# Kernel optimization log

Measured on AMD Instinct MI355X. Metric: run time of the kernel, lower is better.

Reference implementation:

```python
import jax, jax.numpy as jnp
import numpy as np

M, N = 128, 128          # SOM grid
NITER = 1000             # total training iterations
ALPHA = 0.3              # base learning rate (torch default)
SIGMA = max(M, N) / 2.0  # base neighbourhood radius (torch default)
BS, DIM = 4096, 768


def setup_inputs() -> dict:
    key = jax.random.key(0)
    k1, k2 = jax.random.split(key)
    embedded = jax.random.normal(k1, (BS, DIM), dtype=jnp.float32)   # SapBERT CLS reps
    weights = jax.random.normal(k2, (M * N, DIM), dtype=jnp.float32)  # codebook / SOM weights
    return {"embedded": embedded, "weights": weights, "it": 100}


def reference(embedded, weights, it):
    comps = weights.shape[0]
    # neuron grid locations [comps, 2] (row-major i,j like neuron_locations())
    locs = jnp.stack(
        jnp.meshgrid(jnp.arange(M), jnp.arange(N), indexing="ij"), axis=-1
    ).reshape(comps, 2).astype(jnp.float32)

    # BMU search: squared Euclidean distances (argmin identical to argmin of sqrt)
    # [bs, comps] — avoids materializing the torch [bs, comps, dim] repeat
    d2 = (
        jnp.sum(embedded * embedded, axis=1)[:, None]
        + jnp.sum(weights * weights, axis=1)[None, :]
        - 2.0 * (embedded @ weights.T)
    )
    bmu_index = jnp.argmin(d2, axis=1)          # [bs]
    bmu_loc = locs[bmu_index]                   # [bs, 2] gather

    # linearly decaying learning rate / sigma
    decay = 1.0 - it / NITER
    alpha_op = ALPHA * decay
    sigma_op = SIGMA * decay

    # Gaussian neighbourhood over grid distances [bs, comps]
    grid_d2 = jnp.sum((locs[None, :, :] - bmu_loc[:, None, :]) ** 2, axis=-1)
    lr = alpha_op * jnp.exp(-grid_d2 / (sigma_op * sigma_op))

    # delta[c,d] = sum_b lr[b,c] * (x[b,d] - w[c,d])  (no bs x comps x dim materialization)
    delta = jnp.einsum("bc,bd->cd", lr, embedded) - jnp.sum(lr, axis=0)[:, None] * weights
    return weights + delta
```

## Files before the change

kernel.cpp:

```cpp
#include <hip/hip_runtime.h>
#include <cstdint>
#include <cstddef>

#define BS    4096
#define DIM   768
#define DH    384
#define GM    128
#define GN    128
#define COMPS (GM * GN)
#define NITER_F 1000.0f
#define ALPHA0  0.3f
#define SIGMA0  64.0f

typedef _Float16 half8  __attribute__((ext_vector_type(8)));
typedef _Float16 half4v __attribute__((ext_vector_type(4)));
typedef _Float16 half2v __attribute__((ext_vector_type(2)));
typedef float    floatx4 __attribute__((ext_vector_type(4)));

#define XH_OFF    0UL
#define WH_OFF    (8UL * 1024UL * 1024UL)
#define GQ_OFF    0UL
#define GQ_BYTES  ((size_t)COMPS * DH * 4UL)
#define HQ_OFF    (26UL * 1024UL * 1024UL)
#define ETABH_OFF (44UL * 1024UL * 1024UL)
#define BEST_OFF  ((size_t)COMPS * DIM * 4UL)
#define BEST_BYTES ((size_t)BS * 8UL)
#define CNT_OFF   (BEST_OFF + BEST_BYTES)
#define CNT_BYTES ((size_t)COMPS * 4UL)
#define CNTH_OFF  (CNT_OFF + CNT_BYTES)
#define S_OFF     (CNTH_OFF + CNT_BYTES)
#define ETAB_OFF  (S_OFF + CNT_BYTES)
#define WN2_OFF   (ETAB_OFF + CNT_BYTES)

#define GPTR(p) ((const __attribute__((address_space(1))) void*)(p))
#define LPTR(p) ((__attribute__((address_space(3))) void*)(p))

__device__ __forceinline__ unsigned long long packScore(float s, int c) {
    unsigned u = __float_as_uint(s);
    u = (u & 0x80000000u) ? ~u : (u | 0x80000000u);
    return ((unsigned long long)u << 32) | (unsigned)(~(unsigned)c);
}

__device__ __forceinline__ unsigned long long shfl_xor_u64(unsigned long long v, int m) {
    unsigned lo = (unsigned)v, hi = (unsigned)(v >> 32);
    lo = (unsigned)__shfl_xor((int)lo, m, 64);
    hi = (unsigned)__shfl_xor((int)hi, m, 64);
    return ((unsigned long long)hi << 32) | lo;
}

__global__ void cvt_kernel(const float* __restrict__ src, _Float16* __restrict__ dst, int n4) {
    int i = blockIdx.x * 256 + threadIdx.x;
    if (i >= n4) return;
    float4 v = ((const float4*)src)[i];
    half4v h;
    h[0] = (_Float16)v.x; h[1] = (_Float16)v.y;
    h[2] = (_Float16)v.z; h[3] = (_Float16)v.w;
    ((half4v*)dst)[i] = h;
}

__global__ __launch_bounds__(192) void cvtw_wn2_kernel(
    const float* __restrict__ w, _Float16* __restrict__ wh, float* __restrict__ wn2) {
    const int c = blockIdx.x;
    const int t = threadIdx.x;
    const size_t i4 = (size_t)c * 192 + t;
    float4 v = ((const float4*)w)[i4];
    half4v h;
    h[0] = (_Float16)v.x; h[1] = (_Float16)v.y;
    h[2] = (_Float16)v.z; h[3] = (_Float16)v.w;
    ((half4v*)wh)[i4] = h;
    float s = v.x * v.x + v.y * v.y + v.z * v.z + v.w * v.w;
    #pragma unroll
    for (int off = 32; off; off >>= 1) s += __shfl_down(s, off, 64);
    __shared__ float p[3];
    if ((t & 63) == 0) p[t >> 6] = s;
    __syncthreads();
    if (t == 0) wn2[c] = 0.5f * (p[0] + p[1] + p[2]);
}

__global__ void etab_kernel(const int* __restrict__ itp, float* __restrict__ etab,
                            _Float16* __restrict__ etab_h) {
    const int idx = blockIdx.x * 256 + threadIdx.x;
    const int p = idx >> 7, r = idx & 127;
    const float decay = 1.f - (float)(*itp) / NITER_F;
    const float sig = SIGMA0 * decay;
    const float d = (float)(p - r);
    const float v = expf(-(d * d) / (sig * sig));
    etab[idx] = v;
    etab_h[idx] = (_Float16)v;
}

__global__ __launch_bounds__(256) void bmu_kernel(
    const _Float16* __restrict__ xh, const _Float16* __restrict__ wh,
    const float* __restrict__ wn2, unsigned long long* __restrict__ best) {
    __shared__ _Float16 xs[128 * 32];
    __shared__ _Float16 wsd[128 * 32];
    __shared__ unsigned long long red[128];

    const int tid  = threadIdx.x;
    const int wv   = tid >> 6;
    const int lane = tid & 63;
    const int c0 = blockIdx.x * 128;
    const int b0 = blockIdx.y * 128;

    if (tid < 128) red[tid] = 0ULL;

    floatx4 acc[4][4];
    #pragma unroll
    for (int i = 0; i < 4; ++i)
        #pragma unroll
        for (int j = 0; j < 4; ++j) acc[i][j] = (floatx4){0.f, 0.f, 0.f, 0.f};

    const int rr   = lane >> 2;
    const int pq   = lane & 3;
    const int kk   = pq ^ ((rr >> 1) & 3);
    const int lk   = kk * 8;
    const int q    = lane >> 4;
    const int l15  = lane & 15;
    const int mrow = (wv >> 1) * 64;
    const int ncol = (wv & 1) * 64;

    for (int k0 = 0; k0 < DIM; k0 += 32) {
        #pragma unroll
        for (int s = 0; s < 2; ++s) {
            const int sub = 2 * wv + s;
            const _Float16* gx = xh + (size_t)(b0 + sub * 16 + rr) * DIM + k0 + lk;
            __builtin_amdgcn_global_load_lds(GPTR(gx), LPTR(xs + sub * 512), 16, 0, 0);
            const _Float16* gw = wh + (size_t)(c0 + sub * 16 + rr) * DIM + k0 + lk;
            __builtin_amdgcn_global_load_lds(GPTR(gw), LPTR(wsd + sub * 512), 16, 0, 0);
        }
        __syncthreads();

        half8 af[4], bf[4];
        #pragma unroll
        for (int i = 0; i < 4; ++i) {
            const int row = mrow + i * 16 + l15;
            af[i] = *(const half8*)(xs + row * 32 + (q ^ ((row >> 1) & 3)) * 8);
        }
        #pragma unroll
        for (int j = 0; j < 4; ++j) {
            const int row = ncol + j * 16 + l15;
            bf[j] = *(const half8*)(wsd + row * 32 + (q ^ ((row >> 1) & 3)) * 8);
        }
        #pragma unroll
        for (int i = 0; i < 4; ++i)
            #pragma unroll
            for (int j = 0; j < 4; ++j)
                acc[i][j] = __builtin_amdgcn_mfma_f32_16x16x32_f16(af[i], bf[j], acc[i][j], 0, 0, 0);
        __syncthreads();
    }

    float wnj[4];
    #pragma unroll
    for (int j = 0; j < 4; ++j) wnj[j] = wn2[c0 + ncol + j * 16 + l15];

    #pragma unroll
    for (int i = 0; i < 4; ++i) {
        #pragma unroll
        for (int r = 0; r < 4; ++r) {
            unsigned long long m = 0ULL;
            #pragma unroll
            for (int j = 0; j < 4; ++j) {
                float s = acc[i][j][r] - wnj[j];
                unsigned long long p = packScore(s, c0 + ncol + j * 16 + l15);
                if (p > m) m = p;
            }
            #pragma unroll
            for (int msk = 1; msk <= 8; msk <<= 1) {
                unsigned long long o = shfl_xor_u64(m, msk);
                if (o > m) m = o;
            }
            if (l15 == 0)
                atomicMax(&red[mrow + i * 16 + q * 4 + r], m);
        }
    }
    __syncthreads();
    if (tid < 128) atomicMax(&best[b0 + tid], red[tid]);
}

__global__ void scatter_kernel(const unsigned long long* __restrict__ best,
                               const float* __restrict__ x,
                               float* __restrict__ Gq, float* __restrict__ cnt,
                               int h, int addcnt) {
    const int b = blockIdx.x;
    const int c = (int)(~(unsigned)(best[b] & 0xFFFFFFFFULL));
    float* gr = Gq + (size_t)c * DH;
    const float* xr = x + (size_t)b * DIM + h * DH;
    for (int d = threadIdx.x; d < DH; d += 128) atomicAdd(&gr[d], xr[d]);
    if (threadIdx.x == 0 && addcnt) atomicAdd(&cnt[c], 1.0f);
}

#define EP 136
#define BP 40

__global__ __launch_bounds__(256) void convA_kernel(
    const float* __restrict__ Gq, _Float16* __restrict__ H,
    const _Float16* __restrict__ eh) {
    __shared__ _Float16 Es[128 * EP];
    __shared__ _Float16 Bs[128 * BP];
    const int dt = blockIdx.x;
    const int ib = blockIdx.y;
    const int d0 = dt * 128;
    const int tid = threadIdx.x;
    const int wv = tid >> 6, lane = tid & 63;
    const int l15 = lane & 15, q = lane >> 4;
    const int mrow = (wv >> 1) * 64, ncol = (wv & 1) * 64;

    {
        const int row = tid >> 1, hh = tid & 1;
        const _Float16* src = eh + row * 128 + hh * 64;
        _Float16* dst = Es + row * EP + hh * 64;
        #pragma unroll
        for (int u = 0; u < 8; ++u) *(half8*)(dst + u * 8) = *(const half8*)(src + u * 8);
    }

    floatx4 acc[4][4];
    #pragma unroll
    for (int i = 0; i < 4; ++i)
        #pragma unroll
        for (int j = 0; j < 4; ++j) acc[i][j] = (floatx4){0.f, 0.f, 0.f, 0.f};

    const int jj2 = (tid & 15) * 2;
    const int dd  = (tid >> 4) * 8;
    for (int k0 = 0; k0 < 128; k0 += 32) {
        __syncthreads();
        {
            const float* r0 = Gq + (size_t)(ib * 128 + k0 + jj2) * DH + d0 + dd;
            const float* r1 = r0 + DH;
            float4 a0 = *(const float4*)r0, a1 = *(const float4*)(r0 + 4);
            float4 b0 = *(const float4*)r1, b1 = *(const float4*)(r1 + 4);
            float va[8] = {a0.x, a0.y, a0.z, a0.w, a1.x, a1.y, a1.z, a1.w};
            float vb[8] = {b0.x, b0.y, b0.z, b0.w, b1.x, b1.y, b1.z, b1.w};
            #pragma unroll
            for (int u = 0; u < 8; ++u)
                *(half2v*)(Bs + (dd + u) * BP + jj2) = (half2v){(_Float16)va[u], (_Float16)vb[u]};
        }
        __syncthreads();
        half8 af[4], bf[4];
        #pragma unroll
        for (int i = 0; i < 4; ++i)
            af[i] = *(const half8*)(Es + (mrow + i * 16 + l15) * EP + k0 + q * 8);
        #pragma unroll
        for (int j = 0; j < 4; ++j)
            bf[j] = *(const half8*)(Bs + (ncol + j * 16 + l15) * BP + q * 8);
        #pragma unroll
        for (int i = 0; i < 4; ++i)
            #pragma unroll
            for (int j = 0; j < 4; ++j)
                acc[i][j] = __builtin_amdgcn_mfma_f32_16x16x32_f16(af[i], bf[j], acc[i][j], 0, 0, 0);
    }
    __syncthreads();
    #pragma unroll
    for (int i = 0; i < 4; ++i)
        #pragma unroll
        for (int j = 0; j < 4; ++j)
            #pragma unroll
            for (int r = 0; r < 4; ++r)
                Es[(mrow + i * 16 + q * 4 + r) * EP + ncol + j * 16 + l15] = (_Float16)acc[i][j][r];
    __syncthreads();
    {
        const int row = tid >> 1, hh = tid & 1;
        const _Float16* src = Es + row * EP + hh * 64;
        _Float16* dst = H + ((size_t)ib * 128 + row) * DH + d0 + hh * 64;
        #pragma unroll
        for (int u = 0; u < 8; ++u) *(half8*)(dst + u * 8) = *(const half8*)(src + u * 8);
    }
}

__global__ __launch_bounds__(256) void convB_kernel(
    const _Float16* __restrict__ H, const float* __restrict__ w,
    const float* __restrict__ S, const _Float16* __restrict__ eh,
    const int* __restrict__ itp, float* __restrict__ out, int h) {
    __shared__ _Float16 Es[128 * EP];
    __shared__ _Float16 Bs[128 * BP];
    const int dt = blockIdx.x;
    const int jc = blockIdx.y;
    const int d0 = dt * 128;
    const int tid = threadIdx.x;
    const int wv = tid >> 6, lane = tid & 63;
    const int l15 = lane & 15, q = lane >> 4;
    const int mrow = (wv >> 1) * 64, ncol = (wv & 1) * 64;
    const float alpha = ALPHA0 * (1.f - (float)(*itp) / NITER_F);

    {
        const int row = tid >> 1, hh = tid & 1;
        const _Float16* src = eh + row * 128 + hh * 64;
        _Float16* dst = Es + row * EP + hh * 64;
        #pragma unroll
        for (int u = 0; u < 8; ++u) *(half8*)(dst + u * 8) = *(const half8*)(src + u * 8);
    }

    floatx4 acc[4][4];
    #pragma unroll
    for (int i = 0; i < 4; ++i)
        #pragma unroll
        for (int j = 0; j < 4; ++j) acc[i][j] = (floatx4){0.f, 0.f, 0.f, 0.f};

    const int jj2 = (tid & 15) * 2;
    const int dd  = (tid >> 4) * 8;
    for (int k0 = 0; k0 < 128; k0 += 32) {
        __syncthreads();
        {
            const _Float16* r0 = H + ((size_t)(k0 + jj2) * 128 + jc) * DH + d0 + dd;
            const _Float16* r1 = r0 + (size_t)128 * DH;
            half8 a = *(const half8*)r0;
            half8 b = *(const half8*)r1;
            #pragma unroll
            for (int u = 0; u < 8; ++u)
                *(half2v*)(Bs + (dd + u) * BP + jj2) = (half2v){a[u], b[u]};
        }
        __syncthreads();
        half8 af[4], bf[4];
        #pragma unroll
        for (int i = 0; i < 4; ++i)
            af[i] = *(const half8*)(Es + (mrow + i * 16 + l15) * EP + k0 + q * 8);
        #pragma unroll
        for (int j = 0; j < 4; ++j)
            bf[j] = *(const half8*)(Bs + (ncol + j * 16 + l15) * BP + q * 8);
        #pragma unroll
        for (int i = 0; i < 4; ++i)
            #pragma unroll
            for (int j = 0; j < 4; ++j)
                acc[i][j] = __builtin_amdgcn_mfma_f32_16x16x32_f16(af[i], bf[j], acc[i][j], 0, 0, 0);
    }
    __syncthreads();
    float* Ebf = (float*)Es;
    #pragma unroll
    for (int ch = 0; ch < 2; ++ch) {
        if ((wv >> 1) == ch) {
            #pragma unroll
            for (int i = 0; i < 4; ++i)
                #pragma unroll
                for (int j = 0; j < 4; ++j)
                    #pragma unroll
                    for (int r = 0; r < 4; ++r)
                        Ebf[(i * 16 + q * 4 + r) * 132 + ncol + j * 16 + l15] = acc[i][j][r];
        }
        __syncthreads();
        {
            const int row = tid >> 2, seg = tid & 3;
            const int m = ch * 64 + row;
            const int c = m * 128 + jc;
            const float scl = 1.f - alpha * S[c];
            const size_t g = (size_t)c * DIM + h * DH + d0 + seg * 32;
            #pragma unroll
            for (int u = 0; u < 8; ++u) {
                float4 wv4 = *(const float4*)(w + g + u * 4);
                float4 t4  = *(const float4*)(Ebf + row * 132 + seg * 32 + u * 4);
                float4 o;
                o.x = wv4.x * scl + alpha * t4.x;
                o.y = wv4.y * scl + alpha * t4.y;
                o.z = wv4.z * scl + alpha * t4.z;
                o.w = wv4.w * scl + alpha * t4.w;
                *(float4*)(out + g + u * 4) = o;
            }
        }
        __syncthreads();
    }
}

__global__ void cntconv1(const float* __restrict__ cnt, const float* __restrict__ etab,
                         float* __restrict__ cntH) {
    const int idx = blockIdx.x * 256 + threadIdx.x;
    const int i = idx >> 7, jc = idx & 127;
    float s = 0.f;
    for (int j = 0; j < 128; ++j) s += etab[jc * 128 + j] * cnt[i * 128 + j];
    cntH[idx] = s;
}
__global__ void cntconv2(const float* __restrict__ cntH, const float* __restrict__ etab,
                         float* __restrict__ S) {
    const int idx = blockIdx.x * 256 + threadIdx.x;
    const int ic = idx >> 7, jc = idx & 127;
    float s = 0.f;
    for (int i = 0; i < 128; ++i) s += etab[ic * 128 + i] * cntH[i * 128 + jc];
    S[idx] = s;
}

extern "C" void kernel_launch(void* const* d_in, const int* in_sizes, int n_in,
                              void* d_out, int out_size, void* d_ws, size_t ws_size,
                              hipStream_t stream) {
    const float* x  = (const float*)d_in[0];
    const float* w  = (const float*)d_in[1];
    const int* itp  = (const int*)d_in[2];
    float* out = (float*)d_out;
    char* ws = (char*)d_ws;

    _Float16* xh = (_Float16*)(ws + XH_OFF);
    _Float16* wh = (_Float16*)(ws + WH_OFF);
    float*    Gq = (float*)(ws + GQ_OFF);
    _Float16* Hq = (_Float16*)(ws + HQ_OFF);
    _Float16* eh = (_Float16*)(ws + ETABH_OFF);
    unsigned long long* best = (unsigned long long*)(ws + BEST_OFF);
    float* cnt  = (float*)(ws + CNT_OFF);
    float* cntH = (float*)(ws + CNTH_OFF);
    float* S    = (float*)(ws + S_OFF);
    float* etab = (float*)(ws + ETAB_OFF);
    float* wn2  = (float*)(ws + WN2_OFF);

    hipMemsetAsync(ws + BEST_OFF, 0, BEST_BYTES + CNT_BYTES, stream);

    cvt_kernel<<<(BS * DIM / 4 + 255) / 256, 256, 0, stream>>>(x, xh, BS * DIM / 4);
    cvtw_wn2_kernel<<<COMPS, 192, 0, stream>>>(w, wh, wn2);
    etab_kernel<<<COMPS / 256, 256, 0, stream>>>(itp, etab, eh);

    bmu_kernel<<<dim3(COMPS / 128, BS / 128), 256, 0, stream>>>(xh, wh, wn2, best);

    for (int h = 0; h < 2; ++h) {
        hipMemsetAsync(ws + GQ_OFF, 0, GQ_BYTES, stream);
        scatter_kernel<<<BS, 128, 0, stream>>>(best, x, Gq, cnt, h, h == 0 ? 1 : 0);
        if (h == 0) {
            cntconv1<<<COMPS / 256, 256, 0, stream>>>(cnt, etab, cntH);
            cntconv2<<<COMPS / 256, 256, 0, stream>>>(cntH, etab, S);
        }
        convA_kernel<<<dim3(3, 128), 256, 0, stream>>>(Gq, Hq, eh);
        convB_kernel<<<dim3(3, 128), 256, 0, stream>>>(Hq, w, S, eh, itp, out, h);
    }
}
```

Measured before the change: 360.7 us.

## Process full feature dimension in one pass and compute Gaussian table inline

Replaces the two half-dimension passes (scatter, convA, convB per half) with a single pass over all 768 features, accumulating G at full width and using the output buffer as fp32 scratch for the intermediate H. The etab kernel is removed and the Gaussian neighbourhood weights are recomputed with __expf inside convA, convB and the count convolutions. This cuts launches and memsets and doubles the grid width per convolution. In exchange, H is stored in fp32 instead of fp16, doubling its traffic, and convB reads and writes the same buffer, which relies on each block reading only its own column rows before overwriting them.

```diff
diff --git a/kernel.cpp b/kernel.cpp
--- a/kernel.cpp
+++ b/kernel.cpp
@@ -4,7 +4,6 @@
 
 #define BS    4096
 #define DIM   768
-#define DH    384
 #define GM    128
 #define GN    128
 #define COMPS (GM * GN)
@@ -19,18 +18,15 @@
 
 #define XH_OFF    0UL
 #define WH_OFF    (8UL * 1024UL * 1024UL)
-#define GQ_OFF    0UL
-#define GQ_BYTES  ((size_t)COMPS * DH * 4UL)
-#define HQ_OFF    (26UL * 1024UL * 1024UL)
-#define ETABH_OFF (44UL * 1024UL * 1024UL)
-#define BEST_OFF  ((size_t)COMPS * DIM * 4UL)
+#define G_OFF     0UL
+#define G_BYTES   ((size_t)COMPS * DIM * 4UL)
+#define BEST_OFF  G_BYTES
 #define BEST_BYTES ((size_t)BS * 8UL)
 #define CNT_OFF   (BEST_OFF + BEST_BYTES)
 #define CNT_BYTES ((size_t)COMPS * 4UL)
 #define CNTH_OFF  (CNT_OFF + CNT_BYTES)
 #define S_OFF     (CNTH_OFF + CNT_BYTES)
-#define ETAB_OFF  (S_OFF + CNT_BYTES)
-#define WN2_OFF   (ETAB_OFF + CNT_BYTES)
+#define WN2_OFF   (S_OFF + CNT_BYTES)
 
 #define GPTR(p) ((const __attribute__((address_space(1))) void*)(p))
 #define LPTR(p) ((__attribute__((address_space(3))) void*)(p))
@@ -77,18 +73,6 @@
     if (t == 0) wn2[c] = 0.5f * (p[0] + p[1] + p[2]);
 }
 
-__global__ void etab_kernel(const int* __restrict__ itp, float* __restrict__ etab,
-                            _Float16* __restrict__ etab_h) {
-    const int idx = blockIdx.x * 256 + threadIdx.x;
-    const int p = idx >> 7, r = idx & 127;
-    const float decay = 1.f - (float)(*itp) / NITER_F;
-    const float sig = SIGMA0 * decay;
-    const float d = (float)(p - r);
-    const float v = expf(-(d * d) / (sig * sig));
-    etab[idx] = v;
-    etab_h[idx] = (_Float16)v;
-}
-
 __global__ __launch_bounds__(256) void bmu_kernel(
     const _Float16* __restrict__ xh, const _Float16* __restrict__ wh,
     const float* __restrict__ wn2, unsigned long long* __restrict__ best) {
@@ -179,38 +163,44 @@
 
 __global__ void scatter_kernel(const unsigned long long* __restrict__ best,
                                const float* __restrict__ x,
-                               float* __restrict__ Gq, float* __restrict__ cnt,
-                               int h, int addcnt) {
+                               float* __restrict__ G, float* __restrict__ cnt) {
     const int b = blockIdx.x;
     const int c = (int)(~(unsigned)(best[b] & 0xFFFFFFFFULL));
-    float* gr = Gq + (size_t)c * DH;
-    const float* xr = x + (size_t)b * DIM + h * DH;
-    for (int d = threadIdx.x; d < DH; d += 128) atomicAdd(&gr[d], xr[d]);
-    if (threadIdx.x == 0 && addcnt) atomicAdd(&cnt[c], 1.0f);
+    float* gr = G + (size_t)c * DIM;
+    const float* xr = x + (size_t)b * DIM;
+    #pragma unroll
+    for (int u = 0; u < 3; ++u) {
+        const int d = threadIdx.x + u * 256;
+        atomicAdd(&gr[d], xr[d]);
+    }
+    if (threadIdx.x == 0) atomicAdd(&cnt[c], 1.0f);
 }
 
 #define EP 136
 #define BP 40
 
 __global__ __launch_bounds__(256) void convA_kernel(
-    const float* __restrict__ Gq, _Float16* __restrict__ H,
-    const _Float16* __restrict__ eh) {
+    const float* __restrict__ G, float* __restrict__ H, const int* __restrict__ itp) {
     __shared__ _Float16 Es[128 * EP];
     __shared__ _Float16 Bs[128 * BP];
-    const int dt = blockIdx.x;
+    const int d0 = blockIdx.x * 128;
     const int ib = blockIdx.y;
-    const int d0 = dt * 128;
     const int tid = threadIdx.x;
     const int wv = tid >> 6, lane = tid & 63;
     const int l15 = lane & 15, q = lane >> 4;
     const int mrow = (wv >> 1) * 64, ncol = (wv & 1) * 64;
 
     {
+        const float decay = 1.f - (float)(*itp) / NITER_F;
+        const float sig = SIGMA0 * decay;
+        const float inv = -1.f / (sig * sig);
         const int row = tid >> 1, hh = tid & 1;
-        const _Float16* src = eh + row * 128 + hh * 64;
         _Float16* dst = Es + row * EP + hh * 64;
         #pragma unroll
-        for (int u = 0; u < 8; ++u) *(half8*)(dst + u * 8) = *(const half8*)(src + u * 8);
+        for (int u = 0; u < 64; ++u) {
+            const float dd = (float)(row - hh * 64 - u);
+            dst[u] = (_Float16)__expf(dd * dd * inv);
+        }
     }
 
     floatx4 acc[4][4];
@@ -224,8 +214,8 @@
     for (int k0 = 0; k0 < 128; k0 += 32) {
         __syncthreads();
         {
-            const float* r0 = Gq + (size_t)(ib * 128 + k0 + jj2) * DH + d0 + dd;
-            const float* r1 = r0 + DH;
+            const float* r0 = G + (size_t)(ib * 128 + k0 + jj2) * DIM + d0 + dd;
+            const float* r1 = r0 + DIM;
             float4 a0 = *(const float4*)r0, a1 = *(const float4*)(r0 + 4);
             float4 b0 = *(const float4*)r1, b1 = *(const float4*)(r1 + 4);
             float va[8] = {a0.x, a0.y, a0.z, a0.w, a1.x, a1.y, a1.z, a1.w};
@@ -233,80 +223,6 @@
             #pragma unroll
             for (int u = 0; u < 8; ++u)
                 *(half2v*)(Bs + (dd + u) * BP + jj2) = (half2v){(_Float16)va[u], (_Float16)vb[u]};
-        }
-        __syncthreads();
-        half8 af[4], bf[4];
-        #pragma unroll
-        for (int i = 0; i < 4; ++i)
-            af[i] = *(const half8*)(Es + (mrow + i * 16 + l15) * EP + k0 + q * 8);
-        #pragma unroll
-        for (int j = 0; j < 4; ++j)
-            bf[j] = *(const half8*)(Bs + (ncol + j * 16 + l15) * BP + q * 8);
-        #pragma unroll
-        for (int i = 0; i < 4; ++i)
-            #pragma unroll
-            for (int j = 0; j < 4; ++j)
-                acc[i][j] = __builtin_amdgcn_mfma_f32_16x16x32_f16(af[i], bf[j], acc[i][j], 0, 0, 0);
-    }
-    __syncthreads();
-    #pragma unroll
-    for (int i = 0; i < 4; ++i)
-        #pragma unroll
-        for (int j = 0; j < 4; ++j)
-            #pragma unroll
-            for (int r = 0; r < 4; ++r)
-                Es[(mrow + i * 16 + q * 4 + r) * EP + ncol + j * 16 + l15] = (_Float16)acc[i][j][r];
-    __syncthreads();
-    {
-        const int row = tid >> 1, hh = tid & 1;
-        const _Float16* src = Es + row * EP + hh * 64;
-        _Float16* dst = H + ((size_t)ib * 128 + row) * DH + d0 + hh * 64;
-        #pragma unroll
-        for (int u = 0; u < 8; ++u) *(half8*)(dst + u * 8) = *(const half8*)(src + u * 8);
-    }
-}
-
-__global__ __launch_bounds__(256) void convB_kernel(
-    const _Float16* __restrict__ H, const float* __restrict__ w,
-    const float* __restrict__ S, const _Float16* __restrict__ eh,
-    const int* __restrict__ itp, float* __restrict__ out, int h) {
-    __shared__ _Float16 Es[128 * EP];
-    __shared__ _Float16 Bs[128 * BP];
-    const int dt = blockIdx.x;
-    const int jc = blockIdx.y;
-    const int d0 = dt * 128;
-    const int tid = threadIdx.x;
-    const int wv = tid >> 6, lane = tid & 63;
-    const int l15 = lane & 15, q = lane >> 4;
-    const int mrow = (wv >> 1) * 64, ncol = (wv & 1) * 64;
-    const float alpha = ALPHA0 * (1.f - (float)(*itp) / NITER_F);
-
-    {
-        const int row = tid >> 1, hh = tid & 1;
-        const _Float16* src = eh + row * 128 + hh * 64;
-        _Float16* dst = Es + row * EP + hh * 64;
-        #pragma unroll
-        for (int u = 0; u < 8; ++u) *(half8*)(dst + u * 8) = *(const half8*)(src + u * 8);
-    }
-
-    floatx4 acc[4][4];
-    #pragma unroll
-    for (int i = 0; i < 4; ++i)
-        #pragma unroll
-        for (int j = 0; j < 4; ++j) acc[i][j] = (floatx4){0.f, 0.f, 0.f, 0.f};
-
-    const int jj2 = (tid & 15) * 2;
-    const int dd  = (tid >> 4) * 8;
-    for (int k0 = 0; k0 < 128; k0 += 32) {
-        __syncthreads();
-        {
-            const _Float16* r0 = H + ((size_t)(k0 + jj2) * 128 + jc) * DH + d0 + dd;
-            const _Float16* r1 = r0 + (size_t)128 * DH;
-            half8 a = *(const half8*)r0;
-            half8 b = *(const half8*)r1;
-            #pragma unroll
-            for (int u = 0; u < 8; ++u)
-                *(half2v*)(Bs + (dd + u) * BP + jj2) = (half2v){a[u], b[u]};
         }
         __syncthreads();
         half8 af[4], bf[4];
@@ -339,9 +255,96 @@
         {
             const int row = tid >> 2, seg = tid & 3;
             const int m = ch * 64 + row;
+            const size_t g = (size_t)(ib * 128 + m) * DIM + d0 + seg * 32;
+            #pragma unroll
+            for (int u = 0; u < 8; ++u)
+                *(float4*)(H + g + u * 4) = *(const float4*)(Ebf + row * 132 + seg * 32 + u * 4);
+        }
+        __syncthreads();
+    }
+}
+
+__global__ __launch_bounds__(256) void convB_kernel(
+    const float* H, const float* __restrict__ w,
+    const float* __restrict__ S, const int* __restrict__ itp, float* out) {
+    __shared__ _Float16 Es[128 * EP];
+    __shared__ _Float16 Bs[128 * BP];
+    const int d0 = blockIdx.x * 128;
+    const int jc = blockIdx.y;
+    const int tid = threadIdx.x;
+    const int wv = tid >> 6, lane = tid & 63;
+    const int l15 = lane & 15, q = lane >> 4;
+    const int mrow = (wv >> 1) * 64, ncol = (wv & 1) * 64;
+    const float alpha = ALPHA0 * (1.f - (float)(*itp) / NITER_F);
+
+    {
+        const float decay = 1.f - (float)(*itp) / NITER_F;
+        const float sig = SIGMA0 * decay;
+        const float inv = -1.f / (sig * sig);
+        const int row = tid >> 1, hh = tid & 1;
+        _Float16* dst = Es + row * EP + hh * 64;
+        #pragma unroll
+        for (int u = 0; u < 64; ++u) {
+            const float dd = (float)(row - hh * 64 - u);
+            dst[u] = (_Float16)__expf(dd * dd * inv);
+        }
+    }
+
+    floatx4 acc[4][4];
+    #pragma unroll
+    for (int i = 0; i < 4; ++i)
+        #pragma unroll
+        for (int j = 0; j < 4; ++j) acc[i][j] = (floatx4){0.f, 0.f, 0.f, 0.f};
+
+    const int jj2 = (tid & 15) * 2;
+    const int dd  = (tid >> 4) * 8;
+    for (int k0 = 0; k0 < 128; k0 += 32) {
+        __syncthreads();
+        {
+            const float* r0 = H + (size_t)((k0 + jj2) * 128 + jc) * DIM + d0 + dd;
+            const float* r1 = r0 + (size_t)128 * DIM;
+            float4 a0 = *(const float4*)r0, a1 = *(const float4*)(r0 + 4);
+            float4 b0 = *(const float4*)r1, b1 = *(const float4*)(r1 + 4);
+            float va[8] = {a0.x, a0.y, a0.z, a0.w, a1.x, a1.y, a1.z, a1.w};
+            float vb[8] = {b0.x, b0.y, b0.z, b0.w, b1.x, b1.y, b1.z, b1.w};
+            #pragma unroll
+            for (int u = 0; u < 8; ++u)
+                *(half2v*)(Bs + (dd + u) * BP + jj2) = (half2v){(_Float16)va[u], (_Float16)vb[u]};
+        }
+        __syncthreads();
+        half8 af[4], bf[4];
+        #pragma unroll
+        for (int i = 0; i < 4; ++i)
+            af[i] = *(const half8*)(Es + (mrow + i * 16 + l15) * EP + k0 + q * 8);
+        #pragma unroll
+        for (int j = 0; j < 4; ++j)
+            bf[j] = *(const half8*)(Bs + (ncol + j * 16 + l15) * BP + q * 8);
+        #pragma unroll
+        for (int i = 0; i < 4; ++i)
+            #pragma unroll
+            for (int j = 0; j < 4; ++j)
+                acc[i][j] = __builtin_amdgcn_mfma_f32_16x16x32_f16(af[i], bf[j], acc[i][j], 0, 0, 0);
+    }
+    __syncthreads();
+    float* Ebf = (float*)Es;
+    #pragma unroll
+    for (int ch = 0; ch < 2; ++ch) {
+        if ((wv >> 1) == ch) {
+            #pragma unroll
+            for (int i = 0; i < 4; ++i)
+                #pragma unroll
+                for (int j = 0; j < 4; ++j)
+                    #pragma unroll
+                    for (int r = 0; r < 4; ++r)
+                        Ebf[(i * 16 + q * 4 + r) * 132 + ncol + j * 16 + l15] = acc[i][j][r];
+        }
+        __syncthreads();
+        {
+            const int row = tid >> 2, seg = tid & 3;
+            const int m = ch * 64 + row;
             const int c = m * 128 + jc;
             const float scl = 1.f - alpha * S[c];
-            const size_t g = (size_t)c * DIM + h * DH + d0 + seg * 32;
+            const size_t g = (size_t)c * DIM + d0 + seg * 32;
             #pragma unroll
             for (int u = 0; u < 8; ++u) {
                 float4 wv4 = *(const float4*)(w + g + u * 4);
@@ -358,20 +361,32 @@
     }
 }
 
-__global__ void cntconv1(const float* __restrict__ cnt, const float* __restrict__ etab,
-                         float* __restrict__ cntH) {
+__global__ void cntconv1(const float* __restrict__ cnt, float* __restrict__ cntH,
+                         const int* __restrict__ itp) {
     const int idx = blockIdx.x * 256 + threadIdx.x;
     const int i = idx >> 7, jc = idx & 127;
+    const float decay = 1.f - (float)(*itp) / NITER_F;
+    const float sig = SIGMA0 * decay;
+    const float inv = -1.f / (sig * sig);
     float s = 0.f;
-    for (int j = 0; j < 128; ++j) s += etab[jc * 128 + j] * cnt[i * 128 + j];
+    for (int j = 0; j < 128; ++j) {
+        const float dd = (float)(jc - j);
+        s += __expf(dd * dd * inv) * cnt[i * 128 + j];
+    }
     cntH[idx] = s;
 }
-__global__ void cntconv2(const float* __restrict__ cntH, const float* __restrict__ etab,
-                         float* __restrict__ S) {
+__global__ void cntconv2(const float* __restrict__ cntH, float* __restrict__ S,
+                         const int* __restrict__ itp) {
     const int idx = blockIdx.x * 256 + threadIdx.x;
     const int ic = idx >> 7, jc = idx & 127;
+    const float decay = 1.f - (float)(*itp) / NITER_F;
+    const float sig = SIGMA0 * decay;
+    const float inv = -1.f / (sig * sig);
     float s = 0.f;
-    for (int i = 0; i < 128; ++i) s += etab[ic * 128 + i] * cntH[i * 128 + jc];
+    for (int i = 0; i < 128; ++i) {
+        const float dd = (float)(ic - i);
+        s += __expf(dd * dd * inv) * cntH[i * 128 + jc];
+    }
     S[idx] = s;
 }
 
@@ -386,32 +401,26 @@
 
     _Float16* xh = (_Float16*)(ws + XH_OFF);
     _Float16* wh = (_Float16*)(ws + WH_OFF);
-    float*    Gq = (float*)(ws + GQ_OFF);
-    _Float16* Hq = (_Float16*)(ws + HQ_OFF);
-    _Float16* eh = (_Float16*)(ws + ETABH_OFF);
+    float*    G  = (float*)(ws + G_OFF);
     unsigned long long* best = (unsigned long long*)(ws + BEST_OFF);
     float* cnt  = (float*)(ws + CNT_OFF);
     float* cntH = (float*)(ws + CNTH_OFF);
     float* S    = (float*)(ws + S_OFF);
-    float* etab = (float*)(ws + ETAB_OFF);
     float* wn2  = (float*)(ws + WN2_OFF);
 
     hipMemsetAsync(ws + BEST_OFF, 0, BEST_BYTES + CNT_BYTES, stream);
 
     cvt_kernel<<<(BS * DIM / 4 + 255) / 256, 256, 0, stream>>>(x, xh, BS * DIM / 4);
     cvtw_wn2_kernel<<<COMPS, 192, 0, stream>>>(w, wh, wn2);
-    etab_kernel<<<COMPS / 256, 256, 0, stream>>>(itp, etab, eh);
 
     bmu_kernel<<<dim3(COMPS / 128, BS / 128), 256, 0, stream>>>(xh, wh, wn2, best);
 
-    for (int h = 0; h < 2; ++h) {
-        hipMemsetAsync(ws + GQ_OFF, 0, GQ_BYTES, stream);
-        scatter_kernel<<<BS, 128, 0, stream>>>(best, x, Gq, cnt, h, h == 0 ? 1 : 0);
-        if (h == 0) {
-            cntconv1<<<COMPS / 256, 256, 0, stream>>>(cnt, etab, cntH);
-            cntconv2<<<COMPS / 256, 256, 0, stream>>>(cntH, etab, S);
-        }
-        convA_kernel<<<dim3(3, 128), 256, 0, stream>>>(Gq, Hq, eh);
-        convB_kernel<<<dim3(3, 128), 256, 0, stream>>>(Hq, w, S, eh, itp, out, h);
-    }
-}
+    hipMemsetAsync(ws + G_OFF, 0, G_BYTES, stream);
+    scatter_kernel<<<BS, 256, 0, stream>>>(best, x, G, cnt);
+
+    cntconv1<<<COMPS / 256, 256, 0, stream>>>(cnt, cntH, itp);
+    cntconv2<<<COMPS / 256, 256, 0, stream>>>(cntH, S, itp);
+
+    convA_kernel<<<dim3(6, 128), 256, 0, stream>>>(G, out, itp);
+    convB_kernel<<<dim3(6, 128), 256, 0, stream>>>(out, w, S, itp, out);
+}
```

New measurement: 346.9 us. 1.04x faster.
